# Performance work log

Hardware: AMD Instinct MI355X
Metric: run time of the kernel (lower is better)

## Reference

```python
import jax, jax.numpy as jnp
import numpy as np


def setup_inputs() -> dict:
    key = jax.random.key(0)
    ks = jax.random.split(key, 9)
    B, C, H, W = 8, 512, 56, 56
    E = 256  # embed_dim = in_channels / r
    s = 0.02
    return {
        "x": jax.random.normal(ks[0], (B, C, H, W), dtype=jnp.float32),
        "wq": jax.random.normal(ks[1], (E, C), dtype=jnp.float32) * s,
        "bq": jax.random.normal(ks[2], (E,), dtype=jnp.float32) * s,
        "wk": jax.random.normal(ks[3], (E, C), dtype=jnp.float32) * s,
        "bk": jax.random.normal(ks[4], (E,), dtype=jnp.float32) * s,
        "wv": jax.random.normal(ks[5], (E, C), dtype=jnp.float32) * s,
        "bv": jax.random.normal(ks[6], (E,), dtype=jnp.float32) * s,
        "wo": jax.random.normal(ks[7], (C, E), dtype=jnp.float32) * s,
        "bo": jax.random.normal(ks[8], (C,), dtype=jnp.float32) * s,
    }


def reference(x, wq, bq, wk, bk, wv, bv, wo, bo):
    B, C, H, W = x.shape
    N = H * W
    # 1x1 convs == per-pixel linear projections; flatten spatial dims
    xf = x.reshape(B, C, N)                                   # b c n
    q = jnp.einsum("ec,bcn->bne", wq, xf) + bq                # b n e
    k = jnp.einsum("ec,bcn->ben", wk, xf) + bk[None, :, None] # b e n
    v = jnp.einsum("ec,bcn->bne", wv, xf) + bv                # b n e
    attn = jnp.einsum("bne,bem->bnm", q, k) / N               # b n n (unnormalized, /N scale)
    embed = jnp.einsum("bnm,bme->bne", attn, v)               # b n e
    out = jnp.einsum("ce,bne->bcn", wo, embed) + bo[None, :, None]
    return out.reshape(B, C, H, W) + x
```

## Files before the change

kernel.cpp:

```cpp
#include <hip/hip_runtime.h>
#include <hip/hip_bf16.h>


typedef __attribute__((ext_vector_type(8))) __bf16 bf16x8;
typedef __attribute__((ext_vector_type(4))) float floatx4;

struct __align__(8) bh4 { __hip_bfloat16 x, y, z, w; };
struct __align__(16) bh8 { __hip_bfloat16 h[8]; };

__device__ __forceinline__ void load_lds16(const void* g, void* l) {
    __builtin_amdgcn_global_load_lds((const __attribute__((address_space(1))) void*)g,
                                     (__attribute__((address_space(3))) void*)l, 16, 0, 0);
}

__global__ __launch_bounds__(256)
void prep_all(const float* __restrict__ wo, const float* __restrict__ wv,
              const float* __restrict__ wq, const float* __restrict__ wk,
              const float* __restrict__ bq, const float* __restrict__ bk,
              const float* __restrict__ bv,
              __hip_bfloat16* __restrict__ Pdb, __hip_bfloat16* __restrict__ Qtb,
              float* __restrict__ u, float* __restrict__ r, float* __restrict__ w,
              float* __restrict__ kap, float* __restrict__ sv)
{
    const int tid = threadIdx.x;
    if (blockIdx.z == 2) {
        int blk = blockIdx.y * 8 + blockIdx.x;
        if (blk < 2) {
            int c = blk * 256 + tid;
            float su = 0.f, sr = 0.f, sw = 0.f;
            for (int e = 0; e < 256; ++e) {
                su = fmaf(wo[(long long)c * 256 + e], bv[e], su);
                sr = fmaf(bk[e], wq[(long long)e * 512 + c], sr);
                sw = fmaf(wk[(long long)e * 512 + c], bq[e], sw);
            }
            u[c] = su; r[c] = sr; w[c] = sw;
            if (c == 0) {
                float k2 = 0.f;
                for (int e = 0; e < 256; ++e) k2 = fmaf(bk[e], bq[e], k2);
                *kap = k2;
            }
        } else if (blk == 2) {
            float4* p = (float4*)sv;
            for (int i = tid; i < 1024; i += 256) p[i] = make_float4(0.f, 0.f, 0.f, 0.f);
        }
        return;
    }
    __shared__ __align__(16) float As[16][68];
    __shared__ __align__(16) float Bs[16][68];
    const int tx = tid & 15, ty = tid >> 4;
    const int m0 = blockIdx.y * 64, n0 = blockIdx.x * 64;
    const bool doQ = (blockIdx.z == 1);
    const int lk = tid >> 4, lc = (tid & 15) * 4;
    const int lr = tid >> 2, lk4 = (tid & 3) * 4;
    float acc[4][4] = {};
    for (int k0 = 0; k0 < 256; k0 += 16) {
        float4 av, bv4;
        if (doQ) {
            av = *(const float4*)&wq[(long long)(k0 + lk) * 512 + m0 + lc];
            bv4 = *(const float4*)&wk[(long long)(k0 + lk) * 512 + n0 + lc];
        } else {
            av = *(const float4*)&wo[(long long)(m0 + lr) * 256 + k0 + lk4];
            bv4 = *(const float4*)&wv[(long long)(k0 + lk) * 512 + n0 + lc];
        }
        __syncthreads();
        if (doQ) {
            *(float4*)&As[lk][lc] = av;
        } else {
            As[lk4 + 0][lr] = av.x; As[lk4 + 1][lr] = av.y;
            As[lk4 + 2][lr] = av.z; As[lk4 + 3][lr] = av.w;
        }
        *(float4*)&Bs[lk][lc] = bv4;
        __syncthreads();
#pragma unroll
        for (int kk = 0; kk < 16; ++kk) {
            float a[4], b[4];
#pragma unroll
            for (int i = 0; i < 4; ++i) { a[i] = As[kk][ty * 4 + i]; b[i] = Bs[kk][tx * 4 + i]; }
#pragma unroll
            for (int i = 0; i < 4; ++i)
#pragma unroll
                for (int j = 0; j < 4; ++j) acc[i][j] = fmaf(a[i], b[j], acc[i][j]);
        }
    }
    const int mo = m0 + ty * 4, no = n0 + tx * 4;
    if (doQ) {
#pragma unroll
        for (int i = 0; i < 4; ++i)
#pragma unroll
            for (int j = 0; j < 4; ++j)
                Qtb[(long long)(mo + i) * 512 + no + j] = __float2bfloat16(acc[i][j]);
    } else {
#pragma unroll
        for (int i = 0; i < 4; ++i)
#pragma unroll
            for (int j = 0; j < 4; ++j) {
                __hip_bfloat16 v = __float2bfloat16(acc[i][j]);
                Pdb[(long long)(mo + i) * 1024 + no + j] = v;
                Pdb[(long long)(mo + i) * 1024 + no + j + 512] = v;
            }
    }
}

__global__ __launch_bounds__(256)
void transpose_conv(const float* __restrict__ x, __hip_bfloat16* __restrict__ xT,
                    __hip_bfloat16* __restrict__ xnp, float* __restrict__ s)
{
    __shared__ float t[64][65];
    const int b = blockIdx.z;
    const int n0 = blockIdx.x * 64, c0 = blockIdx.y * 64;
    const int tid = threadIdx.x;
    const int nch = tid & 7;
    const int cr  = tid >> 3;
    __hip_bfloat16* xTo = xT + (long long)b * 3200 * 512;
    __hip_bfloat16* xno = xnp + (long long)b * 512 * 3200;

    if (n0 >= 3136) {
        bh8 z8;
#pragma unroll
        for (int k = 0; k < 8; ++k) z8.h[k] = __float2bfloat16(0.f);
#pragma unroll
        for (int pass = 0; pass < 2; ++pass) {
            int rr = cr + 32 * pass;
            *(bh8*)&xno[(long long)(c0 + rr) * 3200 + n0 + nch * 8] = z8;
            *(bh8*)&xTo[(long long)(n0 + rr) * 512 + c0 + nch * 8] = z8;
        }
        return;
    }
    const float* xb = x + (long long)b * 512 * 3136;
#pragma unroll
    for (int pass = 0; pass < 2; ++pass) {
        const int cl = cr + 32 * pass;
        const int c = c0 + cl;
        const float* xr = xb + (long long)c * 3136 + n0 + nch * 8;
        float4 v0 = *(const float4*)xr;
        float4 v1 = *(const float4*)(xr + 4);
        bh8 o;
        o.h[0] = __float2bfloat16(v0.x); o.h[1] = __float2bfloat16(v0.y);
        o.h[2] = __float2bfloat16(v0.z); o.h[3] = __float2bfloat16(v0.w);
        o.h[4] = __float2bfloat16(v1.x); o.h[5] = __float2bfloat16(v1.y);
        o.h[6] = __float2bfloat16(v1.z); o.h[7] = __float2bfloat16(v1.w);
        *(bh8*)&xno[(long long)c * 3200 + n0 + nch * 8] = o;
        const int nl = nch * 8;
        t[nl + 0][cl] = v0.x; t[nl + 1][cl] = v0.y;
        t[nl + 2][cl] = v0.z; t[nl + 3][cl] = v0.w;
        t[nl + 4][cl] = v1.x; t[nl + 5][cl] = v1.y;
        t[nl + 6][cl] = v1.z; t[nl + 7][cl] = v1.w;
        float rs = v0.x + v0.y + v0.z + v0.w + v1.x + v1.y + v1.z + v1.w;
        rs += __shfl_xor(rs, 1, 8);
        rs += __shfl_xor(rs, 2, 8);
        rs += __shfl_xor(rs, 4, 8);
        if (nch == 0) atomicAdd(&s[b * 512 + c], rs);
    }
    __syncthreads();
#pragma unroll
    for (int pass = 0; pass < 2; ++pass) {
        const int nl = cr + 32 * pass;
        const int cc = nch * 8;
        bh8 o;
#pragma unroll
        for (int k = 0; k < 8; ++k) o.h[k] = __float2bfloat16(t[nl][cc + k]);
        *(bh8*)&xTo[(long long)(n0 + nl) * 512 + c0 + cc] = o;
    }
}

__global__ __launch_bounds__(256)
void vec2_kernel(const __hip_bfloat16* __restrict__ T, const __hip_bfloat16* __restrict__ Pdb,
                 const __hip_bfloat16* __restrict__ Qtb, const float* __restrict__ s,
                 const float* __restrict__ u, const float* __restrict__ w,
                 const float* __restrict__ kap, const float* __restrict__ bo,
                 float* __restrict__ ps, float* __restrict__ sq, float* __restrict__ a2)
{
    const int idx = blockIdx.x * 4 + (threadIdx.x >> 6);
    const int lane = threadIdx.x & 63;
    const int b = idx >> 9, c = idx & 511;
    const int j0 = lane * 8;
    const float* sb = s + b * 512;
    float4 s0 = *(const float4*)&sb[j0], s1 = *(const float4*)&sb[j0 + 4];
    float4 w0 = *(const float4*)&w[j0],  w1 = *(const float4*)&w[j0 + 4];
    bf16x8 pv = *(const bf16x8*)&Pdb[(long long)c * 1024 + j0];
    bf16x8 qv = *(const bf16x8*)&Qtb[(long long)c * 512 + j0];
    bf16x8 tv = *(const bf16x8*)&T[(long long)b * 262144 + (long long)c * 512 + j0];
    float sj[8] = {s0.x, s0.y, s0.z, s0.w, s1.x, s1.y, s1.z, s1.w};
    float wj[8] = {w0.x, w0.y, w0.z, w0.w, w1.x, w1.y, w1.z, w1.w};
    float aps = 0.f, asq = 0.f, atw = 0.f, asw = 0.f;
#pragma unroll
    for (int t = 0; t < 8; ++t) {
        aps = fmaf((float)pv[t], sj[t], aps);
        asq = fmaf((float)qv[t], sj[t], asq);
        atw = fmaf((float)tv[t], wj[t], atw);
        asw = fmaf(sj[t], wj[t], asw);
    }
#pragma unroll
    for (int m = 1; m < 64; m <<= 1) {
        aps += __shfl_xor(aps, m);
        asq += __shfl_xor(asq, m);
        atw += __shfl_xor(atw, m);
        asw += __shfl_xor(asw, m);
    }
    if (lane == 0) {
        ps[idx] = aps; sq[idx] = asq;
        float kp = *kap;
        a2[idx] = (atw + u[c] * asw + aps * kp) * (1.f / 3136.f) + u[c] * kp + bo[c];
    }
}

#define SWZ64(row) ((row) & 7)

__global__ __launch_bounds__(256)
void mfma_g(const __hip_bfloat16* __restrict__ A, long long sA, int lda,
            __hip_bfloat16* __restrict__ C, long long sC, int ldc,
            int kLen)
{
    constexpr int BKT = 64;
    constexpr int CPR = BKT / 8;
    constexpr int NC = 64 * CPR / 256;
    __shared__ __hip_bfloat16 As[64 * BKT];
    __shared__ __hip_bfloat16 Bs[64 * BKT];
    const int tid = threadIdx.x;
    const int lane = tid & 63;
    const int w = tid >> 6;
    const int wm = (w >> 1) << 5;
    const int wn = (w & 1) << 5;
    const int ln = lane & 15;
    const int hi = lane >> 4;
    const int bx = blockIdx.x;
    const int batch = bx & 7, ks = bx >> 3;
    int p = blockIdx.y, mt = 0;
    while (p >= 8 - mt) { p -= 8 - mt; ++mt; }
    const int nt = mt + p;
    const int m0 = mt << 6, n0 = nt << 6;
    const long long k0 = (long long)ks * kLen;

    const __hip_bfloat16* gA[NC];
    const __hip_bfloat16* gB[NC];
#pragma unroll
    for (int q0 = 0; q0 < NC; ++q0) {
        int q = tid + 256 * q0;
        int row = q / CPR;
        int c = (q % CPR) ^ SWZ64(row);
        gA[q0] = A + batch * sA + (long long)(m0 + row) * lda + k0 + c * 8;
        gB[q0] = A + batch * sA + (long long)(n0 + row) * lda + k0 + c * 8;
    }
    floatx4 acc[2][2] = {};
    const int nK = kLen / BKT;
    for (int kt = 0; kt < nK; ++kt) {
#pragma unroll
        for (int q0 = 0; q0 < NC; ++q0) {
            load_lds16(gA[q0], As + (tid + 256 * q0) * 8);
            load_lds16(gB[q0], Bs + (tid + 256 * q0) * 8);
            gA[q0] += BKT; gB[q0] += BKT;
        }
        __syncthreads();
#pragma unroll
        for (int kk = 0; kk < BKT / 32; ++kk) {
            const int cidx = kk * 4 + hi;
            bf16x8 af[2], bfr[2];
#pragma unroll
            for (int i = 0; i < 2; ++i) {
                int row = wm + i * 16 + ln;
                af[i] = *(const bf16x8*)(As + row * BKT + ((cidx ^ SWZ64(row)) << 3));
            }
#pragma unroll
            for (int j = 0; j < 2; ++j) {
                int row = wn + j * 16 + ln;
                bfr[j] = *(const bf16x8*)(Bs + row * BKT + ((cidx ^ SWZ64(row)) << 3));
            }
#pragma unroll
            for (int i = 0; i < 2; ++i)
#pragma unroll
                for (int j = 0; j < 2; ++j)
                    acc[i][j] = __builtin_amdgcn_mfma_f32_16x16x32_bf16(af[i], bfr[j], acc[i][j], 0, 0, 0);
        }
        __syncthreads();
    }

    __hip_bfloat16* Cb = C + batch * sC + ks * 512;
#pragma unroll
    for (int i = 0; i < 2; ++i) {
        int mb = m0 + wm + i * 16 + hi * 4;
#pragma unroll
        for (int j = 0; j < 2; ++j) {
            int nl = n0 + wn + j * 16 + ln;
            bh4 mv;
            mv.x = __float2bfloat16(acc[i][j][0]);
            mv.y = __float2bfloat16(acc[i][j][1]);
            mv.z = __float2bfloat16(acc[i][j][2]);
            mv.w = __float2bfloat16(acc[i][j][3]);
            Cb[(long long)(mb + 0) * ldc + nl] = mv.x;
            Cb[(long long)(mb + 1) * ldc + nl] = mv.y;
            Cb[(long long)(mb + 2) * ldc + nl] = mv.z;
            Cb[(long long)(mb + 3) * ldc + nl] = mv.w;
            if (mt != nt)
                *(bh4*)&Cb[(long long)nl * ldc + mb] = mv;
        }
    }
}

template<int MODE>
__global__ __launch_bounds__(256)
void mfma_sm(const __hip_bfloat16* __restrict__ A, long long sA, int lda,
             const __hip_bfloat16* __restrict__ B, long long sB, int ldb,
             __hip_bfloat16* __restrict__ C, long long sC, int ldc,
             const float* __restrict__ pu, const float* __restrict__ pr,
             const float* __restrict__ pps, const float* __restrict__ psq,
             int kLen)
{
    constexpr int BKT = 64;
    constexpr int CPR = BKT / 8;
    constexpr int NC = 64 * CPR / 256;
    __shared__ __hip_bfloat16 As[64 * BKT];
    __shared__ __hip_bfloat16 Bs[64 * BKT];
    const int tid = threadIdx.x;
    const int lane = tid & 63;
    const int w = tid >> 6;
    const int wm = (w >> 1) << 5;
    const int wn = (w & 1) << 5;
    const int ln = lane & 15;
    const int hi = lane >> 4;
    const int batch = blockIdx.x;
    const int m0 = blockIdx.z << 6;
    const int n0 = blockIdx.y << 6;

    const __hip_bfloat16* gA[NC];
    const __hip_bfloat16* gB[NC];
#pragma unroll
    for (int q0 = 0; q0 < NC; ++q0) {
        int q = tid + 256 * q0;
        int row = q / CPR;
        int c = (q % CPR) ^ SWZ64(row);
        gA[q0] = A + batch * sA + (long long)(m0 + row) * lda + c * 8;
        gB[q0] = B + batch * sB + (long long)(n0 + row) * ldb + c * 8;
    }
    floatx4 acc[2][2] = {};
    const int nK = kLen / BKT;
    for (int kt = 0; kt < nK; ++kt) {
#pragma unroll
        for (int q0 = 0; q0 < NC; ++q0) {
            load_lds16(gA[q0], As + (tid + 256 * q0) * 8);
            load_lds16(gB[q0], Bs + (tid + 256 * q0) * 8);
            gA[q0] += BKT; gB[q0] += BKT;
        }
        __syncthreads();
#pragma unroll
        for (int kk = 0; kk < BKT / 32; ++kk) {
            const int cidx = kk * 4 + hi;
            bf16x8 af[2], bfr[2];
#pragma unroll
            for (int i = 0; i < 2; ++i) {
                int row = wm + i * 16 + ln;
                af[i] = *(const bf16x8*)(As + row * BKT + ((cidx ^ SWZ64(row)) << 3));
            }
#pragma unroll
            for (int j = 0; j < 2; ++j) {
                int row = wn + j * 16 + ln;
                bfr[j] = *(const bf16x8*)(Bs + row * BKT + ((cidx ^ SWZ64(row)) << 3));
            }
#pragma unroll
            for (int i = 0; i < 2; ++i)
#pragma unroll
                for (int j = 0; j < 2; ++j)
                    acc[i][j] = __builtin_amdgcn_mfma_f32_16x16x32_bf16(af[i], bfr[j], acc[i][j], 0, 0, 0);
        }
        __syncthreads();
    }

    __hip_bfloat16* Cb = C + batch * sC;
#pragma unroll
    for (int i = 0; i < 2; ++i) {
        int mb = m0 + wm + i * 16 + hi * 4;
#pragma unroll
        for (int r = 0; r < 4; ++r) {
#pragma unroll
            for (int j = 0; j < 2; ++j) {
                int nl = n0 + wn + j * 16 + ln;
                float v = acc[i][j][r];
                if (MODE == 6) {
                    float uu = pu[mb + r], rr = pr[nl];
                    v = (v + uu * psq[batch * 512 + nl] + pps[batch * 512 + mb + r] * rr)
                        * (1.f / 3136.f) + uu * rr;
                }
                Cb[(long long)(mb + r) * ldc + nl] = __float2bfloat16(v);
            }
        }
    }
}

__global__ __launch_bounds__(256)
void mfma64(const __hip_bfloat16* __restrict__ A, long long sA, int lda,
            const __hip_bfloat16* __restrict__ B, long long sB, int ldb,
            float* __restrict__ C, long long sC, int ldc,
            const float* __restrict__ bias, int sBias,
            const float* __restrict__ xres, long long sX,
            int kLen, int Nreal)
{
    constexpr int BKT = 64;
    constexpr int CPR = BKT / 8;
    constexpr int NA = 64 * CPR / 256;
    constexpr int NB = 128 * CPR / 256;
    __shared__ __hip_bfloat16 As[64 * BKT];
    __shared__ __hip_bfloat16 Bs[128 * BKT];
    const int tid = threadIdx.x;
    const int lane = tid & 63;
    const int w = tid >> 6;
    const int ln = lane & 15;
    const int hi = lane >> 4;
    const int batch = blockIdx.x;
    const int m0 = blockIdx.z << 6;
    const int n0 = blockIdx.y << 7;

    const __hip_bfloat16* gA[NA];
    const __hip_bfloat16* gB[NB];
#pragma unroll
    for (int q0 = 0; q0 < NA; ++q0) {
        int q = tid + 256 * q0;
        int row = q / CPR;
        int c = (q % CPR) ^ SWZ64(row);
        gA[q0] = A + batch * sA + (long long)(m0 + row) * lda + c * 8;
    }
#pragma unroll
    for (int q0 = 0; q0 < NB; ++q0) {
        int q = tid + 256 * q0;
        int row = q / CPR;
        int c = (q % CPR) ^ SWZ64(row);
        gB[q0] = B + batch * sB + (long long)(n0 + row) * ldb + c * 8;
    }

    const float* xb = xres + batch * sX;
    float xr[4][4][2];
#pragma unroll
    for (int i = 0; i < 4; ++i)
#pragma unroll
        for (int r = 0; r < 4; ++r)
#pragma unroll
            for (int j = 0; j < 2; ++j) {
                int mb = m0 + i * 16 + hi * 4 + r;
                int nl = n0 + w * 32 + j * 16 + ln;
                int nlc = nl < Nreal ? nl : Nreal - 1;
                xr[i][r][j] = xb[(long long)mb * ldc + nlc];
            }

    floatx4 acc[4][2] = {};
    const int nK = kLen / BKT;
    for (int kt = 0; kt < nK; ++kt) {
#pragma unroll
        for (int q0 = 0; q0 < NA; ++q0) {
            load_lds16(gA[q0], As + (tid + 256 * q0) * 8);
            gA[q0] += BKT;
        }
#pragma unroll
        for (int q0 = 0; q0 < NB; ++q0) {
            load_lds16(gB[q0], Bs + (tid + 256 * q0) * 8);
            gB[q0] += BKT;
        }
        __syncthreads();
#pragma unroll
        for (int kk = 0; kk < BKT / 32; ++kk) {
            const int cidx = kk * 4 + hi;
            bf16x8 af[4], bfr[2];
#pragma unroll
            for (int i = 0; i < 4; ++i) {
                int row = i * 16 + ln;
                af[i] = *(const bf16x8*)(As + row * BKT + ((cidx ^ SWZ64(row)) << 3));
            }
#pragma unroll
            for (int j = 0; j < 2; ++j) {
                int row = w * 32 + j * 16 + ln;
                bfr[j] = *(const bf16x8*)(Bs + row * BKT + ((cidx ^ SWZ64(row)) << 3));
            }
#pragma unroll
            for (int i = 0; i < 4; ++i)
#pragma unroll
                for (int j = 0; j < 2; ++j)
                    acc[i][j] = __builtin_amdgcn_mfma_f32_16x16x32_bf16(af[i], bfr[j], acc[i][j], 0, 0, 0);
        }
        __syncthreads();
    }

    float* Cb = C + batch * sC;
#pragma unroll
    for (int i = 0; i < 4; ++i) {
        int mb = m0 + i * 16 + hi * 4;
#pragma unroll
        for (int r = 0; r < 4; ++r) {
            float bb = bias[batch * sBias + mb + r];
#pragma unroll
            for (int j = 0; j < 2; ++j) {
                int nl = n0 + w * 32 + j * 16 + ln;
                if (nl < Nreal) {
                    Cb[(long long)(mb + r) * ldc + nl] = acc[i][j][r] + bb + xr[i][r][j];
                }
            }
        }
    }
}

extern "C" void kernel_launch(void* const* d_in, const int* in_sizes, int n_in,
                              void* d_out, int out_size, void* d_ws, size_t ws_size,
                              hipStream_t stream)
{
    const float* x  = (const float*)d_in[0];
    const float* wq = (const float*)d_in[1];
    const float* bq = (const float*)d_in[2];
    const float* wk = (const float*)d_in[3];
    const float* bk = (const float*)d_in[4];
    const float* wv = (const float*)d_in[5];
    const float* bv = (const float*)d_in[6];
    const float* wo = (const float*)d_in[7];
    const float* bo = (const float*)d_in[8];
    float* out = (float*)d_out;

    const int N = 3136;
    const long long xs = 512LL * N;
    const long long xs2 = 512LL * 3200;

    char* ob = (char*)d_out;
    __hip_bfloat16* xnp = (__hip_bfloat16*)ob;
    __hip_bfloat16* Gp2 = (__hip_bfloat16*)(ob + 26214400);
    __hip_bfloat16* Tb  = (__hip_bfloat16*)(ob + 34603008);

    char* wsb = (char*)d_ws;
    __hip_bfloat16* xT  = (__hip_bfloat16*)wsb;
    __hip_bfloat16* A2b = (__hip_bfloat16*)(wsb + 26214400);
    __hip_bfloat16* Pdb = (__hip_bfloat16*)(wsb + 30408704);
    __hip_bfloat16* Qtb = (__hip_bfloat16*)(wsb + 31457280);
    float* sv  = (float*)(wsb + 31981568);
    float* u_  = (float*)(wsb + 31997952);
    float* r_  = (float*)(wsb + 32000000);
    float* w_  = (float*)(wsb + 32002048);
    float* kap = (float*)(wsb + 32004096);
    float* ps  = (float*)(wsb + 32004112);
    float* sq  = (float*)(wsb + 32020496);
    float* a2v = (float*)(wsb + 32036880);

    prep_all<<<dim3(8, 8, 3), 256, 0, stream>>>(wo, wv, wq, wk, bq, bk, bv,
                                                Pdb, Qtb, u_, r_, w_, kap, sv);

    transpose_conv<<<dim3(50, 8, 8), 256, 0, stream>>>(x, xT, xnp, sv);

    mfma_g<<<dim3(16, 36), 256, 0, stream>>>(
        xnp, xs2, 3200, Gp2, 524288, 1024, 1600);

    mfma_sm<5><<<dim3(8, 8, 8), 256, 0, stream>>>(
        Pdb, 0, 1024, Gp2, 524288, 1024, Tb, 262144, 512,
        nullptr, nullptr, nullptr, nullptr, 1024);

    vec2_kernel<<<1024, 256, 0, stream>>>(Tb, Pdb, Qtb, sv, u_, w_, kap, bo, ps, sq, a2v);

    mfma_sm<6><<<dim3(8, 8, 8), 256, 0, stream>>>(
        Tb, 262144, 512, Qtb, 0, 512, A2b, 262144, 512,
        u_, r_, ps, sq, 512);

    mfma64<<<dim3(8, 25, 8), 256, 0, stream>>>(
        A2b, 262144, 512, xT, 3200LL * 512, 512,
        out, xs, N, a2v, 512, x, xs, 512, N);
}
```

Baseline: 228.6 us.

## Double-buffer LDS tiles in GEMM kernels to overlap loads with MFMA

The three MFMA GEMM kernels now use two LDS buffers per operand. The next K tile is prefetched with global_load_lds while the current tile is consumed, so each iteration needs one barrier instead of two. In mfma64 the residual x loads are moved into the last iteration so they overlap with the final compute instead of running before the loop. This doubles LDS use per block, which may lower occupancy. The compiler may also insert vmcnt waits that serialize the prefetch anyway.

```diff
diff --git a/kernel.cpp b/kernel.cpp
--- a/kernel.cpp
+++ b/kernel.cpp
@@ -214,8 +214,9 @@
     constexpr int BKT = 64;
     constexpr int CPR = BKT / 8;
     constexpr int NC = 64 * CPR / 256;
-    __shared__ __hip_bfloat16 As[64 * BKT];
-    __shared__ __hip_bfloat16 Bs[64 * BKT];
+    constexpr int LSZ = 64 * BKT;
+    __shared__ __hip_bfloat16 As[2 * LSZ];
+    __shared__ __hip_bfloat16 Bs[2 * LSZ];
     const int tid = threadIdx.x;
     const int lane = tid & 63;
     const int w = tid >> 6;
@@ -243,14 +244,28 @@
     }
     floatx4 acc[2][2] = {};
     const int nK = kLen / BKT;
+
+#pragma unroll
+    for (int q0 = 0; q0 < NC; ++q0) {
+        load_lds16(gA[q0], As + (tid + 256 * q0) * 8);
+        load_lds16(gB[q0], Bs + (tid + 256 * q0) * 8);
+        gA[q0] += BKT; gB[q0] += BKT;
+    }
+    __syncthreads();
+
+    int cur = 0;
     for (int kt = 0; kt < nK; ++kt) {
-#pragma unroll
-        for (int q0 = 0; q0 < NC; ++q0) {
-            load_lds16(gA[q0], As + (tid + 256 * q0) * 8);
-            load_lds16(gB[q0], Bs + (tid + 256 * q0) * 8);
-            gA[q0] += BKT; gB[q0] += BKT;
-        }
-        __syncthreads();
+        if (kt + 1 < nK) {
+            const int off = (cur ^ 1) * LSZ;
+#pragma unroll
+            for (int q0 = 0; q0 < NC; ++q0) {
+                load_lds16(gA[q0], As + off + (tid + 256 * q0) * 8);
+                load_lds16(gB[q0], Bs + off + (tid + 256 * q0) * 8);
+                gA[q0] += BKT; gB[q0] += BKT;
+            }
+        }
+        const __hip_bfloat16* Ac = As + cur * LSZ;
+        const __hip_bfloat16* Bc = Bs + cur * LSZ;
 #pragma unroll
         for (int kk = 0; kk < BKT / 32; ++kk) {
             const int cidx = kk * 4 + hi;
@@ -258,12 +273,12 @@
 #pragma unroll
             for (int i = 0; i < 2; ++i) {
                 int row = wm + i * 16 + ln;
-                af[i] = *(const bf16x8*)(As + row * BKT + ((cidx ^ SWZ64(row)) << 3));
+                af[i] = *(const bf16x8*)(Ac + row * BKT + ((cidx ^ SWZ64(row)) << 3));
             }
 #pragma unroll
             for (int j = 0; j < 2; ++j) {
                 int row = wn + j * 16 + ln;
-                bfr[j] = *(const bf16x8*)(Bs + row * BKT + ((cidx ^ SWZ64(row)) << 3));
+                bfr[j] = *(const bf16x8*)(Bc + row * BKT + ((cidx ^ SWZ64(row)) << 3));
             }
 #pragma unroll
             for (int i = 0; i < 2; ++i)
@@ -271,7 +286,10 @@
                 for (int j = 0; j < 2; ++j)
                     acc[i][j] = __builtin_amdgcn_mfma_f32_16x16x32_bf16(af[i], bfr[j], acc[i][j], 0, 0, 0);
         }
-        __syncthreads();
+        if (kt + 1 < nK) {
+            __syncthreads();
+            cur ^= 1;
+        }
     }
 
     __hip_bfloat16* Cb = C + batch * sC + ks * 512;
@@ -308,8 +326,9 @@
     constexpr int BKT = 64;
     constexpr int CPR = BKT / 8;
     constexpr int NC = 64 * CPR / 256;
-    __shared__ __hip_bfloat16 As[64 * BKT];
-    __shared__ __hip_bfloat16 Bs[64 * BKT];
+    constexpr int LSZ = 64 * BKT;
+    __shared__ __hip_bfloat16 As[2 * LSZ];
+    __shared__ __hip_bfloat16 Bs[2 * LSZ];
     const int tid = threadIdx.x;
     const int lane = tid & 63;
     const int w = tid >> 6;
@@ -333,14 +352,28 @@
     }
     floatx4 acc[2][2] = {};
     const int nK = kLen / BKT;
+
+#pragma unroll
+    for (int q0 = 0; q0 < NC; ++q0) {
+        load_lds16(gA[q0], As + (tid + 256 * q0) * 8);
+        load_lds16(gB[q0], Bs + (tid + 256 * q0) * 8);
+        gA[q0] += BKT; gB[q0] += BKT;
+    }
+    __syncthreads();
+
+    int cur = 0;
     for (int kt = 0; kt < nK; ++kt) {
-#pragma unroll
-        for (int q0 = 0; q0 < NC; ++q0) {
-            load_lds16(gA[q0], As + (tid + 256 * q0) * 8);
-            load_lds16(gB[q0], Bs + (tid + 256 * q0) * 8);
-            gA[q0] += BKT; gB[q0] += BKT;
-        }
-        __syncthreads();
+        if (kt + 1 < nK) {
+            const int off = (cur ^ 1) * LSZ;
+#pragma unroll
+            for (int q0 = 0; q0 < NC; ++q0) {
+                load_lds16(gA[q0], As + off + (tid + 256 * q0) * 8);
+                load_lds16(gB[q0], Bs + off + (tid + 256 * q0) * 8);
+                gA[q0] += BKT; gB[q0] += BKT;
+            }
+        }
+        const __hip_bfloat16* Ac = As + cur * LSZ;
+        const __hip_bfloat16* Bc = Bs + cur * LSZ;
 #pragma unroll
         for (int kk = 0; kk < BKT / 32; ++kk) {
             const int cidx = kk * 4 + hi;
@@ -348,12 +381,12 @@
 #pragma unroll
             for (int i = 0; i < 2; ++i) {
                 int row = wm + i * 16 + ln;
-                af[i] = *(const bf16x8*)(As + row * BKT + ((cidx ^ SWZ64(row)) << 3));
+                af[i] = *(const bf16x8*)(Ac + row * BKT + ((cidx ^ SWZ64(row)) << 3));
             }
 #pragma unroll
             for (int j = 0; j < 2; ++j) {
                 int row = wn + j * 16 + ln;
-                bfr[j] = *(const bf16x8*)(Bs + row * BKT + ((cidx ^ SWZ64(row)) << 3));
+                bfr[j] = *(const bf16x8*)(Bc + row * BKT + ((cidx ^ SWZ64(row)) << 3));
             }
 #pragma unroll
             for (int i = 0; i < 2; ++i)
@@ -361,7 +394,10 @@
                 for (int j = 0; j < 2; ++j)
                     acc[i][j] = __builtin_amdgcn_mfma_f32_16x16x32_bf16(af[i], bfr[j], acc[i][j], 0, 0, 0);
         }
-        __syncthreads();
+        if (kt + 1 < nK) {
+            __syncthreads();
+            cur ^= 1;
+        }
     }
 
     __hip_bfloat16* Cb = C + batch * sC;
@@ -397,8 +433,10 @@
     constexpr int CPR = BKT / 8;
     constexpr int NA = 64 * CPR / 256;
     constexpr int NB = 128 * CPR / 256;
-    __shared__ __hip_bfloat16 As[64 * BKT];
-    __shared__ __hip_bfloat16 Bs[128 * BKT];
+    constexpr int LSA = 64 * BKT;
+    constexpr int LSB = 128 * BKT;
+    __shared__ __hip_bfloat16 As[2 * LSA];
+    __shared__ __hip_bfloat16 Bs[2 * LSB];
     const int tid = threadIdx.x;
     const int lane = tid & 63;
     const int w = tid >> 6;
@@ -427,32 +465,52 @@
 
     const float* xb = xres + batch * sX;
     float xr[4][4][2];
-#pragma unroll
-    for (int i = 0; i < 4; ++i)
-#pragma unroll
-        for (int r = 0; r < 4; ++r)
-#pragma unroll
-            for (int j = 0; j < 2; ++j) {
-                int mb = m0 + i * 16 + hi * 4 + r;
-                int nl = n0 + w * 32 + j * 16 + ln;
-                int nlc = nl < Nreal ? nl : Nreal - 1;
-                xr[i][r][j] = xb[(long long)mb * ldc + nlc];
-            }
 
     floatx4 acc[4][2] = {};
     const int nK = kLen / BKT;
+
+#pragma unroll
+    for (int q0 = 0; q0 < NA; ++q0) {
+        load_lds16(gA[q0], As + (tid + 256 * q0) * 8);
+        gA[q0] += BKT;
+    }
+#pragma unroll
+    for (int q0 = 0; q0 < NB; ++q0) {
+        load_lds16(gB[q0], Bs + (tid + 256 * q0) * 8);
+        gB[q0] += BKT;
+    }
+    __syncthreads();
+
+    int cur = 0;
     for (int kt = 0; kt < nK; ++kt) {
-#pragma unroll
-        for (int q0 = 0; q0 < NA; ++q0) {
-            load_lds16(gA[q0], As + (tid + 256 * q0) * 8);
-            gA[q0] += BKT;
-        }
-#pragma unroll
-        for (int q0 = 0; q0 < NB; ++q0) {
-            load_lds16(gB[q0], Bs + (tid + 256 * q0) * 8);
-            gB[q0] += BKT;
-        }
-        __syncthreads();
+        if (kt + 1 < nK) {
+            const int offA = (cur ^ 1) * LSA;
+            const int offB = (cur ^ 1) * LSB;
+#pragma unroll
+            for (int q0 = 0; q0 < NA; ++q0) {
+                load_lds16(gA[q0], As + offA + (tid + 256 * q0) * 8);
+                gA[q0] += BKT;
+            }
+#pragma unroll
+            for (int q0 = 0; q0 < NB; ++q0) {
+                load_lds16(gB[q0], Bs + offB + (tid + 256 * q0) * 8);
+                gB[q0] += BKT;
+            }
+        } else {
+#pragma unroll
+            for (int i = 0; i < 4; ++i)
+#pragma unroll
+                for (int r = 0; r < 4; ++r)
+#pragma unroll
+                    for (int j = 0; j < 2; ++j) {
+                        int mb = m0 + i * 16 + hi * 4 + r;
+                        int nl = n0 + w * 32 + j * 16 + ln;
+                        int nlc = nl < Nreal ? nl : Nreal - 1;
+                        xr[i][r][j] = xb[(long long)mb * ldc + nlc];
+                    }
+        }
+        const __hip_bfloat16* Ac = As + cur * LSA;
+        const __hip_bfloat16* Bc = Bs + cur * LSB;
 #pragma unroll
         for (int kk = 0; kk < BKT / 32; ++kk) {
             const int cidx = kk * 4 + hi;
@@ -460,12 +518,12 @@
 #pragma unroll
             for (int i = 0; i < 4; ++i) {
                 int row = i * 16 + ln;
-                af[i] = *(const bf16x8*)(As + row * BKT + ((cidx ^ SWZ64(row)) << 3));
+                af[i] = *(const bf16x8*)(Ac + row * BKT + ((cidx ^ SWZ64(row)) << 3));
             }
 #pragma unroll
             for (int j = 0; j < 2; ++j) {
                 int row = w * 32 + j * 16 + ln;
-                bfr[j] = *(const bf16x8*)(Bs + row * BKT + ((cidx ^ SWZ64(row)) << 3));
+                bfr[j] = *(const bf16x8*)(Bc + row * BKT + ((cidx ^ SWZ64(row)) << 3));
             }
 #pragma unroll
             for (int i = 0; i < 4; ++i)
@@ -473,7 +531,10 @@
                 for (int j = 0; j < 2; ++j)
                     acc[i][j] = __builtin_amdgcn_mfma_f32_16x16x32_bf16(af[i], bfr[j], acc[i][j], 0, 0, 0);
         }
-        __syncthreads();
+        if (kt + 1 < nK) {
+            __syncthreads();
+            cur ^= 1;
+        }
     }
 
     float* Cb = C + batch * sC;
```

New measurement: 232.3 us. Within noise of the previous version (+1.6%).
